# Kernel tuning notes

Hardware: AMD Instinct MI355X
Metric: run time of the kernel (lower is better)

Reference implementation:

```python
import jax, jax.numpy as jnp
import numpy as np

N, E, D, R = 8192, 131072, 128, 32
SIZES = (3, 5, 7)  # per-degree component counts (2l+1)
LN_EPS = 1e-5


def setup_inputs() -> dict:
    key = jax.random.key(0)
    ks = jax.random.split(key, 20)
    rn = lambda k, shape, s=1.0: jax.random.normal(k, shape, jnp.float32) * s
    inp = {
        'X0': rn(ks[0], (N, SIZES[0], D)),
        'X1': rn(ks[1], (N, SIZES[1], D)),
        'X2': rn(ks[2], (N, SIZES[2], D)),
        't_ij': rn(ks[3], (E, D)),
        'r0': rn(ks[4], (E, SIZES[0])),
        'r1': rn(ks[5], (E, SIZES[1])),
        'r2': rn(ks[6], (E, SIZES[2])),
        'edge_index': jax.random.randint(ks[7], (2, E), 0, N, dtype=jnp.int32),
        # params
        'W_vq': rn(ks[8], (D, R), D ** -0.5),
        'W_vk0': rn(ks[9], (D, R), D ** -0.5),
        'W_vk1': rn(ks[10], (D, R), D ** -0.5),
        'W_vk2': rn(ks[11], (D, R), D ** -0.5),
        'ln_g': jnp.ones((R,), jnp.float32),
        'ln_b': jnp.zeros((R,), jnp.float32),
        'W_w': rn(ks[12], (R, D), R ** -0.5),
        'b_w': jnp.zeros((D,), jnp.float32),
        'W_t1': rn(ks[13], (D, D), D ** -0.5),
        'b_t1': jnp.zeros((D,), jnp.float32),
        'W_t2': rn(ks[14], (D, D), D ** -0.5),
        'b_t2': jnp.zeros((D,), jnp.float32),
    }
    return inp


def _vec_rej(x, r):
    # x: [E, L, R], r: [E, L]; dot over component dim (L), keepdim, subtract projection
    r = r[..., None]
    dot = jnp.sum(x * r, axis=1, keepdims=True)  # [E, 1, R]
    return x - dot * r


def reference(X0, X1, X2, t_ij, r0, r1, r2, edge_index,
              W_vq, W_vk0, W_vk1, W_vk2, ln_g, ln_b, W_w, b_w,
              W_t1, b_t1, W_t2, b_t2):
    n_j, n_i = edge_index[0], edge_index[1]
    X_ls = jnp.concatenate([X0, X1, X2], axis=1)                 # [N, 15, D]
    eq_i = jnp.einsum('nld,dr->nlr', X_ls, W_vq)[n_i]            # [E, 15, R]
    ek = jnp.concatenate([
        jnp.einsum('nld,dr->nlr', X0, W_vk0),
        jnp.einsum('nld,dr->nlr', X1, W_vk1),
        jnp.einsum('nld,dr->nlr', X2, W_vk2)], axis=1)
    ek_j = ek[n_j]                                               # [E, 15, R]
    # per-degree vector rejection (vec_rej=True)
    qs, ksl, off = [], [], 0
    for r in (r0, r1, r2):
        s = r.shape[1]
        qs.append(_vec_rej(eq_i[:, off:off + s], r))
        ksl.append(_vec_rej(ek_j[:, off:off + s], -r))
        off += s
    eq_i = jnp.concatenate(qs, axis=1)
    ek_j = jnp.concatenate(ksl, axis=1)
    w_ij = jnp.sum(eq_i * ek_j, axis=1)                          # [E, R]
    # mlp_w = LayerNorm + Linear
    mu = jnp.mean(w_ij, axis=-1, keepdims=True)
    var = jnp.var(w_ij, axis=-1, keepdims=True)
    wn = (w_ij - mu) * jax.lax.rsqrt(var + LN_EPS) * ln_g + ln_b
    dw = wn @ W_w + b_w                                          # [E, D]
    # mlp_t = Linear -> silu -> Linear, then outer activation
    t = jax.nn.silu(t_ij @ W_t1 + b_t1) @ W_t2 + b_t2            # [E, D]
    return dw * jax.nn.silu(t)
```

## Files before the change

### kernel.cpp

```cpp
#include <hip/hip_runtime.h>
#include <hip/hip_bf16.h>

#define N_NODES 8192
#define N_EDGES 131072
#define LN_EPS  1e-5f

typedef __attribute__((ext_vector_type(8))) short bf16x8;
typedef __attribute__((ext_vector_type(4))) float f32x4;

__device__ __forceinline__ float silu_f(float x) {
    return x * __builtin_amdgcn_rcpf(1.0f + __expf(-x));
}

__device__ __forceinline__ unsigned short f2bf(float x) {
    union { float f; unsigned int u; } v; v.f = x;
    unsigned int r = v.u + 0x7FFFu + ((v.u >> 16) & 1u);
    return (unsigned short)(r >> 16);
}
__device__ __forceinline__ float bf2f(unsigned short u) {
    union { float f; unsigned int x; } v; v.x = ((unsigned int)u) << 16;
    return v.f;
}
__device__ __forceinline__ unsigned int pk2(float a, float b) {
    float2 t; t.x = a; t.y = b;
    union { __hip_bfloat162 h; unsigned int u; } v;
    v.h = __float22bfloat162_rn(t);
    return v.u;
}
__device__ __forceinline__ bf16x8 pack8(float4 u, float4 v) {
    union { bf16x8 b; unsigned int w[4]; } o;
    o.w[0] = pk2(u.x, u.y); o.w[1] = pk2(u.z, u.w);
    o.w[2] = pk2(v.x, v.y); o.w[3] = pk2(v.z, v.w);
    return o.b;
}
__device__ __forceinline__ f32x4 mfma16(bf16x8 a, bf16x8 b, f32x4 c) {
    return __builtin_amdgcn_mfma_f32_16x16x32_bf16(a, b, c, 0, 0, 0);
}

__global__ __launch_bounds__(256) void prep_kernel(
    const float* __restrict__ W_w, const float* __restrict__ W_t1,
    const float* __restrict__ W_t2, const float* __restrict__ Wvq,
    const float* __restrict__ Wvk0, const float* __restrict__ Wvk1,
    const float* __restrict__ Wvk2,
    unsigned short* __restrict__ Wtw, unsigned short* __restrict__ Wt1b,
    unsigned short* __restrict__ Wt2b, unsigned short* __restrict__ Wqt,
    unsigned short* __restrict__ Wk0t, unsigned short* __restrict__ Wk1t,
    unsigned short* __restrict__ Wk2t)
{
    int i = blockIdx.x * 256 + threadIdx.x;
    if (i < 16384) {
        int n = i >> 7, k = i & 127;
        Wt1b[i] = f2bf(W_t1[k * 128 + n]);
        Wt2b[i] = f2bf(W_t2[k * 128 + n]);
    }
    if (i < 4096) {
        { int n = i >> 5, k = i & 31; Wtw[i] = f2bf(W_w[k * 128 + n]); }
        int r = i >> 7, d = i & 127;
        Wqt[i]  = f2bf(Wvq [d * 32 + r]);
        Wk0t[i] = f2bf(Wvk0[d * 32 + r]);
        Wk1t[i] = f2bf(Wvk1[d * 32 + r]);
        Wk2t[i] = f2bf(Wvk2[d * 32 + r]);
    }
}

template<int S, int LOFF>
__device__ __forceinline__ void proj_body(
    const float* __restrict__ X, const unsigned short* __restrict__ Wqt,
    const unsigned short* __restrict__ Wkt,
    unsigned short* __restrict__ eq, unsigned short* __restrict__ ek,
    int row0)
{
    const int tid  = threadIdx.x;
    const int lane = tid & 63;
    const int wv   = tid >> 6;
    const int l15  = lane & 15;
    const int lk   = lane >> 4;
    const int xrow = row0 + wv * 16 + l15;

    bf16x8 xf[4];
    #pragma unroll
    for (int kt = 0; kt < 4; ++kt) {
        const float* p = X + (size_t)xrow * 128 + kt * 32 + lk * 8;
        xf[kt] = pack8(*(const float4*)p, *(const float4*)(p + 4));
    }

    f32x4 qa[2], ka[2];
    #pragma unroll
    for (int h = 0; h < 2; ++h) {
        qa[h] = (f32x4){0.f, 0.f, 0.f, 0.f};
        ka[h] = (f32x4){0.f, 0.f, 0.f, 0.f};
    }
    #pragma unroll
    for (int kt = 0; kt < 4; ++kt) {
        #pragma unroll
        for (int h = 0; h < 2; ++h) {
            bf16x8 wq = *(const bf16x8*)&Wqt[(h * 16 + l15) * 128 + kt * 32 + lk * 8];
            bf16x8 wk = *(const bf16x8*)&Wkt[(h * 16 + l15) * 128 + kt * 32 + lk * 8];
            qa[h] = mfma16(wq, xf[kt], qa[h]);
            ka[h] = mfma16(wk, xf[kt], ka[h]);
        }
    }

    const int n = xrow / S;
    const int l = xrow % S + LOFF;
    const size_t base = (size_t)n * 512 + l;
    #pragma unroll
    for (int h = 0; h < 2; ++h) {
        #pragma unroll
        for (int j = 0; j < 4; ++j) {
            const int r = h * 16 + lk * 4 + j;
            eq[base + r * 16] = f2bf(qa[h][j]);
            ek[base + r * 16] = f2bf(ka[h][j]);
        }
    }
}

__global__ __launch_bounds__(256) void proj_kernel(
    const float* __restrict__ X0, const float* __restrict__ X1,
    const float* __restrict__ X2,
    const unsigned short* __restrict__ Wqt,
    const unsigned short* __restrict__ Wk0t,
    const unsigned short* __restrict__ Wk1t,
    const unsigned short* __restrict__ Wk2t,
    unsigned short* __restrict__ eq, unsigned short* __restrict__ ek)
{
    const int b = blockIdx.x;
    if (b < 384)
        proj_body<3, 0>(X0, Wqt, Wk0t, eq, ek, b * 64);
    else if (b < 1024)
        proj_body<5, 3>(X1, Wqt, Wk1t, eq, ek, (b - 384) * 64);
    else
        proj_body<7, 8>(X2, Wqt, Wk2t, eq, ek, (b - 1024) * 64);
}

__global__ __launch_bounds__(256) void wn_kernel(
    const unsigned short* __restrict__ eq, const unsigned short* __restrict__ ek,
    const float* __restrict__ r0, const float* __restrict__ r1,
    const float* __restrict__ r2, const int* __restrict__ eidx,
    const float* __restrict__ ln_g, const float* __restrict__ ln_b,
    unsigned short* __restrict__ wn)
{
    const int tid = threadIdx.x;
    const int r   = tid & 31;
    const int e   = blockIdx.x * 8 + (tid >> 5);
    const float g  = ln_g[r];
    const float bb = ln_b[r];
    const int nj = eidx[e];
    const int ni = eidx[N_EDGES + e];

    const unsigned short* qp = eq + (size_t)ni * 512 + r * 16;
    const unsigned short* kp = ek + (size_t)nj * 512 + r * 16;
    bf16x8 q0 = *(const bf16x8*)qp;
    bf16x8 q1 = *(const bf16x8*)(qp + 8);
    bf16x8 k0 = *(const bf16x8*)kp;
    bf16x8 k1 = *(const bf16x8*)(kp + 8);

    float q[15], k[15], rv[15];
    #pragma unroll
    for (int l = 0; l < 8; ++l) {
        q[l] = bf2f((unsigned short)q0[l]);
        k[l] = bf2f((unsigned short)k0[l]);
    }
    #pragma unroll
    for (int l = 8; l < 15; ++l) {
        q[l] = bf2f((unsigned short)q1[l - 8]);
        k[l] = bf2f((unsigned short)k1[l - 8]);
    }
    #pragma unroll
    for (int c = 0; c < 3; ++c) rv[c]     = r0[e * 3 + c];
    #pragma unroll
    for (int c = 0; c < 5; ++c) rv[3 + c] = r1[e * 5 + c];
    #pragma unroll
    for (int c = 0; c < 7; ++c) rv[8 + c] = r2[e * 7 + c];

    float dq, dk;
    dq = q[0]*rv[0] + q[1]*rv[1] + q[2]*rv[2];
    dk = k[0]*rv[0] + k[1]*rv[1] + k[2]*rv[2];
    #pragma unroll
    for (int l = 0; l < 3; ++l) { q[l] -= dq * rv[l]; k[l] -= dk * rv[l]; }
    dq = 0.f; dk = 0.f;
    #pragma unroll
    for (int l = 3; l < 8; ++l) { dq += q[l]*rv[l]; dk += k[l]*rv[l]; }
    #pragma unroll
    for (int l = 3; l < 8; ++l) { q[l] -= dq * rv[l]; k[l] -= dk * rv[l]; }
    dq = 0.f; dk = 0.f;
    #pragma unroll
    for (int l = 8; l < 15; ++l) { dq += q[l]*rv[l]; dk += k[l]*rv[l]; }
    #pragma unroll
    for (int l = 8; l < 15; ++l) { q[l] -= dq * rv[l]; k[l] -= dk * rv[l]; }

    float w = 0.f;
    #pragma unroll
    for (int l = 0; l < 15; ++l) w = fmaf(q[l], k[l], w);

    float s = w, s2 = w * w;
    s += __shfl_xor(s, 1);  s2 += __shfl_xor(s2, 1);
    s += __shfl_xor(s, 2);  s2 += __shfl_xor(s2, 2);
    s += __shfl_xor(s, 4);  s2 += __shfl_xor(s2, 4);
    s += __shfl_xor(s, 8);  s2 += __shfl_xor(s2, 8);
    s += __shfl_xor(s, 16); s2 += __shfl_xor(s2, 16);
    const float mu  = s * (1.f / 32.f);
    const float var = s2 * (1.f / 32.f) - mu * mu;
    const float wnv = (w - mu) * rsqrtf(var + LN_EPS) * g + bb;
    wn[(size_t)e * 32 + r] = f2bf(wnv);
}

__global__ __launch_bounds__(256) void edge_kernel(
    const float* __restrict__ t_ij,
    const unsigned short* __restrict__ wn,
    const unsigned short* __restrict__ Wtw, const float* __restrict__ b_w,
    const unsigned short* __restrict__ Wt1, const float* __restrict__ b_t1,
    const unsigned short* __restrict__ Wt2, const float* __restrict__ b_t2,
    float* __restrict__ out)
{
    __shared__ __align__(16) unsigned short Hp[4][64 * 128];

    const int tid  = threadIdx.x;
    const int lane = tid & 63;
    const int wv   = tid >> 6;
    const int l15  = lane & 15;
    const int lk   = lane >> 4;
    const int tile = (blockIdx.x * 4 + wv) * 64;
    char* hp = (char*)&Hp[wv][0];
    const int swz = (l15 & 7) << 4;

    bf16x8 a1[4][4];
    #pragma unroll
    for (int kt = 0; kt < 4; ++kt)
        #pragma unroll
        for (int rt = 0; rt < 4; ++rt) {
            const float* p = t_ij + (size_t)(tile + rt * 16 + l15) * 128
                           + kt * 32 + lk * 8;
            a1[kt][rt] = pack8(*(const float4*)p, *(const float4*)(p + 4));
        }

    bf16x8 wnf[4];
    #pragma unroll
    for (int rt = 0; rt < 4; ++rt)
        wnf[rt] = *(const bf16x8*)&wn[(size_t)(tile + rt * 16 + l15) * 32 + lk * 8];

    #pragma unroll
    for (int ct = 0; ct < 8; ++ct) {
        bf16x8 w1f[4];
        #pragma unroll
        for (int kt = 0; kt < 4; ++kt)
            w1f[kt] = *(const bf16x8*)&Wt1[(size_t)(ct * 16 + l15) * 128
                                           + kt * 32 + lk * 8];
        f32x4 ac[4];
        #pragma unroll
        for (int rt = 0; rt < 4; ++rt) ac[rt] = (f32x4){0.f, 0.f, 0.f, 0.f};
        #pragma unroll
        for (int kt = 0; kt < 4; ++kt)
            #pragma unroll
            for (int rt = 0; rt < 4; ++rt)
                ac[rt] = mfma16(w1f[kt], a1[kt][rt], ac[rt]);

        const float4 bt1 = *(const float4*)&b_t1[ct * 16 + lk * 4];
        #pragma unroll
        for (int rt = 0; rt < 4; ++rt) {
            uint2 hh;
            hh.x = pk2(silu_f(ac[rt][0] + bt1.x), silu_f(ac[rt][1] + bt1.y));
            hh.y = pk2(silu_f(ac[rt][2] + bt1.z), silu_f(ac[rt][3] + bt1.w));
            *(uint2*)(hp + (((rt * 16 + l15) * 256 + ct * 32 + lk * 8) ^ swz)) = hh;
        }
    }

    bf16x8 a2[4][4];
    #pragma unroll
    for (int kt = 0; kt < 4; ++kt)
        #pragma unroll
        for (int rt = 0; rt < 4; ++rt)
            a2[kt][rt] = *(const bf16x8*)(hp +
                (((rt * 16 + l15) * 256 + kt * 64 + lk * 16) ^ swz));

    #pragma unroll
    for (int ct = 0; ct < 8; ++ct) {
        bf16x8 w2f[4];
        #pragma unroll
        for (int kt = 0; kt < 4; ++kt)
            w2f[kt] = *(const bf16x8*)&Wt2[(size_t)(ct * 16 + l15) * 128
                                           + kt * 32 + lk * 8];
        bf16x8 wwf = *(const bf16x8*)&Wtw[(ct * 16 + l15) * 32 + lk * 8];

        f32x4 o[4], d[4];
        #pragma unroll
        for (int rt = 0; rt < 4; ++rt) o[rt] = (f32x4){0.f, 0.f, 0.f, 0.f};
        #pragma unroll
        for (int kt = 0; kt < 4; ++kt)
            #pragma unroll
            for (int rt = 0; rt < 4; ++rt)
                o[rt] = mfma16(w2f[kt], a2[kt][rt], o[rt]);
        #pragma unroll
        for (int rt = 0; rt < 4; ++rt)
            d[rt] = mfma16(wwf, wnf[rt], (f32x4){0.f, 0.f, 0.f, 0.f});

        const float4 bwv = *(const float4*)&b_w[ct * 16 + lk * 4];
        const float4 b2v = *(const float4*)&b_t2[ct * 16 + lk * 4];
        #pragma unroll
        for (int rt = 0; rt < 4; ++rt) {
            float4 s;
            s.x = (d[rt][0] + bwv.x) * silu_f(o[rt][0] + b2v.x);
            s.y = (d[rt][1] + bwv.y) * silu_f(o[rt][1] + b2v.y);
            s.z = (d[rt][2] + bwv.z) * silu_f(o[rt][2] + b2v.z);
            s.w = (d[rt][3] + bwv.w) * silu_f(o[rt][3] + b2v.w);
            *(float4*)&out[(size_t)(tile + rt * 16 + l15) * 128 + ct * 16 + lk * 4] = s;
        }
    }
}

extern "C" void kernel_launch(void* const* d_in, const int* in_sizes, int n_in,
                              void* d_out, int out_size, void* d_ws, size_t ws_size,
                              hipStream_t stream) {
    (void)in_sizes; (void)n_in; (void)out_size; (void)ws_size;
    const float* X0   = (const float*)d_in[0];
    const float* X1   = (const float*)d_in[1];
    const float* X2   = (const float*)d_in[2];
    const float* t_ij = (const float*)d_in[3];
    const float* r0   = (const float*)d_in[4];
    const float* r1   = (const float*)d_in[5];
    const float* r2   = (const float*)d_in[6];
    const int*   eidx = (const int*)d_in[7];
    const float* Wvq  = (const float*)d_in[8];
    const float* Wvk0 = (const float*)d_in[9];
    const float* Wvk1 = (const float*)d_in[10];
    const float* Wvk2 = (const float*)d_in[11];
    const float* ln_g = (const float*)d_in[12];
    const float* ln_b = (const float*)d_in[13];
    const float* W_w  = (const float*)d_in[14];
    const float* b_w  = (const float*)d_in[15];
    const float* W_t1 = (const float*)d_in[16];
    const float* b_t1 = (const float*)d_in[17];
    const float* W_t2 = (const float*)d_in[18];
    const float* b_t2 = (const float*)d_in[19];
    float* out = (float*)d_out;

    unsigned short* eq   = (unsigned short*)d_ws;
    unsigned short* ek   = eq  + (size_t)N_NODES * 512;
    unsigned short* wn   = ek  + (size_t)N_NODES * 512;
    unsigned short* Wtw  = wn  + (size_t)N_EDGES * 32;
    unsigned short* Wt1b = Wtw  + 4096;
    unsigned short* Wt2b = Wt1b + 16384;
    unsigned short* Wqt  = Wt2b + 16384;
    unsigned short* Wk0t = Wqt  + 4096;
    unsigned short* Wk1t = Wk0t + 4096;
    unsigned short* Wk2t = Wk1t + 4096;

    prep_kernel<<<64, 256, 0, stream>>>(W_w, W_t1, W_t2, Wvq, Wvk0, Wvk1, Wvk2,
                                        Wtw, Wt1b, Wt2b, Wqt, Wk0t, Wk1t, Wk2t);
    proj_kernel<<<1920, 256, 0, stream>>>(X0, X1, X2, Wqt, Wk0t, Wk1t, Wk2t,
                                          eq, ek);
    wn_kernel<<<N_EDGES / 8, 256, 0, stream>>>(eq, ek, r0, r1, r2, eidx,
                                               ln_g, ln_b, wn);
    edge_kernel<<<N_EDGES / 256, 256, 0, stream>>>(t_ij, wn, Wtw, b_w,
                                                   Wt1b, b_t1, Wt2b, b_t2, out);
}
```

Measured before the change: 110.1 us.

## Fuse edge-weight LayerNorm into edge kernel with algebraic rejection and folded affine

Removes the separate wn kernel. Each lane of the edge kernel now gathers its own edge's full q and k rows and computes all 32 channel weights itself. The paired vector rejections are rewritten as qk - dq*dk*(2-|r|^2), so the rejected vectors are never formed. LayerNorm gain and bias are folded into the bf16 W_w matrix and a precomputed bias in the prep kernel. Normalized weights go through LDS into MFMA fragments, which removes the wn round-trip to global memory and one launch. The cost is higher register pressure (32 weights per lane), uncoalesced per-lane row gathers, and a serializing barrier before the t_ij loads.

```diff
diff --git a/kernel.cpp b/kernel.cpp
--- a/kernel.cpp
+++ b/kernel.cpp
@@ -41,11 +41,12 @@
     const float* __restrict__ W_w, const float* __restrict__ W_t1,
     const float* __restrict__ W_t2, const float* __restrict__ Wvq,
     const float* __restrict__ Wvk0, const float* __restrict__ Wvk1,
-    const float* __restrict__ Wvk2,
+    const float* __restrict__ Wvk2, const float* __restrict__ ln_g,
+    const float* __restrict__ ln_b, const float* __restrict__ b_w,
     unsigned short* __restrict__ Wtw, unsigned short* __restrict__ Wt1b,
     unsigned short* __restrict__ Wt2b, unsigned short* __restrict__ Wqt,
     unsigned short* __restrict__ Wk0t, unsigned short* __restrict__ Wk1t,
-    unsigned short* __restrict__ Wk2t)
+    unsigned short* __restrict__ Wk2t, float* __restrict__ bwf)
 {
     int i = blockIdx.x * 256 + threadIdx.x;
     if (i < 16384) {
@@ -54,12 +55,19 @@
         Wt2b[i] = f2bf(W_t2[k * 128 + n]);
     }
     if (i < 4096) {
-        { int n = i >> 5, k = i & 31; Wtw[i] = f2bf(W_w[k * 128 + n]); }
+        { int n = i >> 5, r = i & 31; Wtw[i] = f2bf(ln_g[r] * W_w[r * 128 + n]); }
         int r = i >> 7, d = i & 127;
         Wqt[i]  = f2bf(Wvq [d * 32 + r]);
         Wk0t[i] = f2bf(Wvk0[d * 32 + r]);
         Wk1t[i] = f2bf(Wvk1[d * 32 + r]);
         Wk2t[i] = f2bf(Wvk2[d * 32 + r]);
+    }
+    if (blockIdx.x == 0 && threadIdx.x < 128) {
+        const int n = threadIdx.x;
+        float acc = b_w[n];
+        #pragma unroll
+        for (int r = 0; r < 32; ++r) acc += ln_b[r] * W_w[r * 128 + n];
+        bwf[n] = acc;
     }
 }
 
@@ -133,82 +141,12 @@
         proj_body<7, 8>(X2, Wqt, Wk2t, eq, ek, (b - 1024) * 64);
 }
 
-__global__ __launch_bounds__(256) void wn_kernel(
+__global__ __launch_bounds__(256) void edge_kernel(
+    const float* __restrict__ t_ij,
     const unsigned short* __restrict__ eq, const unsigned short* __restrict__ ek,
     const float* __restrict__ r0, const float* __restrict__ r1,
     const float* __restrict__ r2, const int* __restrict__ eidx,
-    const float* __restrict__ ln_g, const float* __restrict__ ln_b,
-    unsigned short* __restrict__ wn)
-{
-    const int tid = threadIdx.x;
-    const int r   = tid & 31;
-    const int e   = blockIdx.x * 8 + (tid >> 5);
-    const float g  = ln_g[r];
-    const float bb = ln_b[r];
-    const int nj = eidx[e];
-    const int ni = eidx[N_EDGES + e];
-
-    const unsigned short* qp = eq + (size_t)ni * 512 + r * 16;
-    const unsigned short* kp = ek + (size_t)nj * 512 + r * 16;
-    bf16x8 q0 = *(const bf16x8*)qp;
-    bf16x8 q1 = *(const bf16x8*)(qp + 8);
-    bf16x8 k0 = *(const bf16x8*)kp;
-    bf16x8 k1 = *(const bf16x8*)(kp + 8);
-
-    float q[15], k[15], rv[15];
-    #pragma unroll
-    for (int l = 0; l < 8; ++l) {
-        q[l] = bf2f((unsigned short)q0[l]);
-        k[l] = bf2f((unsigned short)k0[l]);
-    }
-    #pragma unroll
-    for (int l = 8; l < 15; ++l) {
-        q[l] = bf2f((unsigned short)q1[l - 8]);
-        k[l] = bf2f((unsigned short)k1[l - 8]);
-    }
-    #pragma unroll
-    for (int c = 0; c < 3; ++c) rv[c]     = r0[e * 3 + c];
-    #pragma unroll
-    for (int c = 0; c < 5; ++c) rv[3 + c] = r1[e * 5 + c];
-    #pragma unroll
-    for (int c = 0; c < 7; ++c) rv[8 + c] = r2[e * 7 + c];
-
-    float dq, dk;
-    dq = q[0]*rv[0] + q[1]*rv[1] + q[2]*rv[2];
-    dk = k[0]*rv[0] + k[1]*rv[1] + k[2]*rv[2];
-    #pragma unroll
-    for (int l = 0; l < 3; ++l) { q[l] -= dq * rv[l]; k[l] -= dk * rv[l]; }
-    dq = 0.f; dk = 0.f;
-    #pragma unroll
-    for (int l = 3; l < 8; ++l) { dq += q[l]*rv[l]; dk += k[l]*rv[l]; }
-    #pragma unroll
-    for (int l = 3; l < 8; ++l) { q[l] -= dq * rv[l]; k[l] -= dk * rv[l]; }
-    dq = 0.f; dk = 0.f;
-    #pragma unroll
-    for (int l = 8; l < 15; ++l) { dq += q[l]*rv[l]; dk += k[l]*rv[l]; }
-    #pragma unroll
-    for (int l = 8; l < 15; ++l) { q[l] -= dq * rv[l]; k[l] -= dk * rv[l]; }
-
-    float w = 0.f;
-    #pragma unroll
-    for (int l = 0; l < 15; ++l) w = fmaf(q[l], k[l], w);
-
-    float s = w, s2 = w * w;
-    s += __shfl_xor(s, 1);  s2 += __shfl_xor(s2, 1);
-    s += __shfl_xor(s, 2);  s2 += __shfl_xor(s2, 2);
-    s += __shfl_xor(s, 4);  s2 += __shfl_xor(s2, 4);
-    s += __shfl_xor(s, 8);  s2 += __shfl_xor(s2, 8);
-    s += __shfl_xor(s, 16); s2 += __shfl_xor(s2, 16);
-    const float mu  = s * (1.f / 32.f);
-    const float var = s2 * (1.f / 32.f) - mu * mu;
-    const float wnv = (w - mu) * rsqrtf(var + LN_EPS) * g + bb;
-    wn[(size_t)e * 32 + r] = f2bf(wnv);
-}
-
-__global__ __launch_bounds__(256) void edge_kernel(
-    const float* __restrict__ t_ij,
-    const unsigned short* __restrict__ wn,
-    const unsigned short* __restrict__ Wtw, const float* __restrict__ b_w,
+    const unsigned short* __restrict__ Wtw, const float* __restrict__ bwf,
     const unsigned short* __restrict__ Wt1, const float* __restrict__ b_t1,
     const unsigned short* __restrict__ Wt2, const float* __restrict__ b_t2,
     float* __restrict__ out)
@@ -224,6 +162,80 @@
     char* hp = (char*)&Hp[wv][0];
     const int swz = (l15 & 7) << 4;
 
+    const int e  = tile + lane;
+    const int nj = eidx[e];
+    const int ni = eidx[N_EDGES + e];
+
+    float rv[15];
+    #pragma unroll
+    for (int c = 0; c < 3; ++c) rv[c]     = r0[e * 3 + c];
+    #pragma unroll
+    for (int c = 0; c < 5; ++c) rv[3 + c] = r1[e * 5 + c];
+    #pragma unroll
+    for (int c = 0; c < 7; ++c) rv[8 + c] = r2[e * 7 + c];
+    float c0 = 2.f, c1 = 2.f, c2 = 2.f;
+    #pragma unroll
+    for (int l = 0; l < 3; ++l)  c0 -= rv[l] * rv[l];
+    #pragma unroll
+    for (int l = 3; l < 8; ++l)  c1 -= rv[l] * rv[l];
+    #pragma unroll
+    for (int l = 8; l < 15; ++l) c2 -= rv[l] * rv[l];
+
+    const unsigned short* qbase = eq + (size_t)ni * 512;
+    const unsigned short* kbase = ek + (size_t)nj * 512;
+
+    float w[32];
+    #pragma unroll
+    for (int r = 0; r < 32; ++r) {
+        bf16x8 q0 = *(const bf16x8*)(qbase + r * 16);
+        bf16x8 q1 = *(const bf16x8*)(qbase + r * 16 + 8);
+        bf16x8 k0 = *(const bf16x8*)(kbase + r * 16);
+        bf16x8 k1 = *(const bf16x8*)(kbase + r * 16 + 8);
+        float qv[15], kv[15];
+        #pragma unroll
+        for (int l = 0; l < 8; ++l) {
+            qv[l] = bf2f((unsigned short)q0[l]);
+            kv[l] = bf2f((unsigned short)k0[l]);
+        }
+        #pragma unroll
+        for (int l = 8; l < 15; ++l) {
+            qv[l] = bf2f((unsigned short)q1[l - 8]);
+            kv[l] = bf2f((unsigned short)k1[l - 8]);
+        }
+        float qk = 0.f;
+        #pragma unroll
+        for (int l = 0; l < 15; ++l) qk = fmaf(qv[l], kv[l], qk);
+        float dq0 = 0.f, dk0 = 0.f, dq1 = 0.f, dk1 = 0.f, dq2 = 0.f, dk2 = 0.f;
+        #pragma unroll
+        for (int l = 0; l < 3; ++l)  { dq0 = fmaf(qv[l], rv[l], dq0); dk0 = fmaf(kv[l], rv[l], dk0); }
+        #pragma unroll
+        for (int l = 3; l < 8; ++l)  { dq1 = fmaf(qv[l], rv[l], dq1); dk1 = fmaf(kv[l], rv[l], dk1); }
+        #pragma unroll
+        for (int l = 8; l < 15; ++l) { dq2 = fmaf(qv[l], rv[l], dq2); dk2 = fmaf(kv[l], rv[l], dk2); }
+        w[r] = qk - dq0 * dk0 * c0 - dq1 * dk1 * c1 - dq2 * dk2 * c2;
+    }
+
+    float s = 0.f, s2 = 0.f;
+    #pragma unroll
+    for (int r = 0; r < 32; ++r) { s += w[r]; s2 += w[r] * w[r]; }
+    const float mu   = s * (1.f / 32.f);
+    const float var  = s2 * (1.f / 32.f) - mu * mu;
+    const float rstd = rsqrtf(var + LN_EPS);
+
+    #pragma unroll
+    for (int p = 0; p < 8; ++p) {
+        uint2 pp;
+        pp.x = pk2((w[4*p+0] - mu) * rstd, (w[4*p+1] - mu) * rstd);
+        pp.y = pk2((w[4*p+2] - mu) * rstd, (w[4*p+3] - mu) * rstd);
+        *(uint2*)(hp + lane * 80 + p * 8) = pp;
+    }
+    bf16x8 wnf[4];
+    #pragma unroll
+    for (int rt = 0; rt < 4; ++rt)
+        wnf[rt] = *(const bf16x8*)(hp + (rt * 16 + l15) * 80 + lk * 16);
+    asm volatile("s_waitcnt lgkmcnt(0)" ::: "memory");
+    __builtin_amdgcn_sched_barrier(0);
+
     bf16x8 a1[4][4];
     #pragma unroll
     for (int kt = 0; kt < 4; ++kt)
@@ -233,11 +245,6 @@
                            + kt * 32 + lk * 8;
             a1[kt][rt] = pack8(*(const float4*)p, *(const float4*)(p + 4));
         }
-
-    bf16x8 wnf[4];
-    #pragma unroll
-    for (int rt = 0; rt < 4; ++rt)
-        wnf[rt] = *(const bf16x8*)&wn[(size_t)(tile + rt * 16 + l15) * 32 + lk * 8];
 
     #pragma unroll
     for (int ct = 0; ct < 8; ++ct) {
@@ -294,16 +301,16 @@
         for (int rt = 0; rt < 4; ++rt)
             d[rt] = mfma16(wwf, wnf[rt], (f32x4){0.f, 0.f, 0.f, 0.f});
 
-        const float4 bwv = *(const float4*)&b_w[ct * 16 + lk * 4];
+        const float4 bwv = *(const float4*)&bwf[ct * 16 + lk * 4];
         const float4 b2v = *(const float4*)&b_t2[ct * 16 + lk * 4];
         #pragma unroll
         for (int rt = 0; rt < 4; ++rt) {
-            float4 s;
-            s.x = (d[rt][0] + bwv.x) * silu_f(o[rt][0] + b2v.x);
-            s.y = (d[rt][1] + bwv.y) * silu_f(o[rt][1] + b2v.y);
-            s.z = (d[rt][2] + bwv.z) * silu_f(o[rt][2] + b2v.z);
-            s.w = (d[rt][3] + bwv.w) * silu_f(o[rt][3] + b2v.w);
-            *(float4*)&out[(size_t)(tile + rt * 16 + l15) * 128 + ct * 16 + lk * 4] = s;
+            float4 so;
+            so.x = (d[rt][0] + bwv.x) * silu_f(o[rt][0] + b2v.x);
+            so.y = (d[rt][1] + bwv.y) * silu_f(o[rt][1] + b2v.y);
+            so.z = (d[rt][2] + bwv.z) * silu_f(o[rt][2] + b2v.z);
+            so.w = (d[rt][3] + bwv.w) * silu_f(o[rt][3] + b2v.w);
+            *(float4*)&out[(size_t)(tile + rt * 16 + l15) * 128 + ct * 16 + lk * 4] = so;
         }
     }
 }
@@ -336,21 +343,22 @@
 
     unsigned short* eq   = (unsigned short*)d_ws;
     unsigned short* ek   = eq  + (size_t)N_NODES * 512;
-    unsigned short* wn   = ek  + (size_t)N_NODES * 512;
-    unsigned short* Wtw  = wn  + (size_t)N_EDGES * 32;
+    unsigned short* Wtw  = ek  + (size_t)N_NODES * 512;
     unsigned short* Wt1b = Wtw  + 4096;
     unsigned short* Wt2b = Wt1b + 16384;
     unsigned short* Wqt  = Wt2b + 16384;
     unsigned short* Wk0t = Wqt  + 4096;
     unsigned short* Wk1t = Wk0t + 4096;
     unsigned short* Wk2t = Wk1t + 4096;
+    float*          bwf  = (float*)(Wk2t + 4096);
 
     prep_kernel<<<64, 256, 0, stream>>>(W_w, W_t1, W_t2, Wvq, Wvk0, Wvk1, Wvk2,
-                                        Wtw, Wt1b, Wt2b, Wqt, Wk0t, Wk1t, Wk2t);
+                                        ln_g, ln_b, b_w,
+                                        Wtw, Wt1b, Wt2b, Wqt, Wk0t, Wk1t, Wk2t,
+                                        bwf);
     proj_kernel<<<1920, 256, 0, stream>>>(X0, X1, X2, Wqt, Wk0t, Wk1t, Wk2t,
                                           eq, ek);
-    wn_kernel<<<N_EDGES / 8, 256, 0, stream>>>(eq, ek, r0, r1, r2, eidx,
-                                               ln_g, ln_b, wn);
-    edge_kernel<<<N_EDGES / 256, 256, 0, stream>>>(t_ij, wn, Wtw, b_w,
+    edge_kernel<<<N_EDGES / 256, 256, 0, stream>>>(t_ij, eq, ek, r0, r1, r2,
+                                                   eidx, Wtw, bwf,
                                                    Wt1b, b_t1, Wt2b, b_t2, out);
 }
```

Result: slower. 121.6 us (+10.5%).

## Use closed-form rejected dot product, two edges per thread, hoist MLP weights

Applied to the files above, without the earlier changes.

Replaces the per-degree vector rejection in wn_kernel with a closed-form expression, qk - (q·r)(k·r)(2-|r|^2), which avoids materialising rejected vectors. Each thread now handles two edges, to raise memory-level parallelism for the gathers, and the grid is halved to match. In edge_kernel, all W_t1 and W_t2 MFMA fragments are preloaded into registers before their loops, and launch bounds are set to two blocks per SM. This increases register pressure and may cause spills. The closed form also rounds slightly differently.

```diff
diff --git a/kernel.cpp b/kernel.cpp
--- a/kernel.cpp
+++ b/kernel.cpp
@@ -133,6 +133,40 @@
         proj_body<7, 8>(X2, Wqt, Wk2t, eq, ek, (b - 1024) * 64);
 }
 
+__device__ __forceinline__ float edge_w(
+    bf16x8 q0, bf16x8 q1, bf16x8 k0, bf16x8 k1, const float* rv)
+{
+    float qv[15], kv[15];
+    #pragma unroll
+    for (int l = 0; l < 8; ++l) {
+        qv[l] = bf2f((unsigned short)q0[l]);
+        kv[l] = bf2f((unsigned short)k0[l]);
+    }
+    #pragma unroll
+    for (int l = 8; l < 15; ++l) {
+        qv[l] = bf2f((unsigned short)q1[l - 8]);
+        kv[l] = bf2f((unsigned short)k1[l - 8]);
+    }
+    float qk = 0.f;
+    #pragma unroll
+    for (int l = 0; l < 15; ++l) qk = fmaf(qv[l], kv[l], qk);
+    float c0 = 2.f, c1 = 2.f, c2 = 2.f;
+    #pragma unroll
+    for (int l = 0; l < 3; ++l)  c0 -= rv[l] * rv[l];
+    #pragma unroll
+    for (int l = 3; l < 8; ++l)  c1 -= rv[l] * rv[l];
+    #pragma unroll
+    for (int l = 8; l < 15; ++l) c2 -= rv[l] * rv[l];
+    float dq0 = 0.f, dk0 = 0.f, dq1 = 0.f, dk1 = 0.f, dq2 = 0.f, dk2 = 0.f;
+    #pragma unroll
+    for (int l = 0; l < 3; ++l)  { dq0 = fmaf(qv[l], rv[l], dq0); dk0 = fmaf(kv[l], rv[l], dk0); }
+    #pragma unroll
+    for (int l = 3; l < 8; ++l)  { dq1 = fmaf(qv[l], rv[l], dq1); dk1 = fmaf(kv[l], rv[l], dk1); }
+    #pragma unroll
+    for (int l = 8; l < 15; ++l) { dq2 = fmaf(qv[l], rv[l], dq2); dk2 = fmaf(kv[l], rv[l], dk2); }
+    return qk - dq0 * dk0 * c0 - dq1 * dk1 * c1 - dq2 * dk2 * c2;
+}
+
 __global__ __launch_bounds__(256) void wn_kernel(
     const unsigned short* __restrict__ eq, const unsigned short* __restrict__ ek,
     const float* __restrict__ r0, const float* __restrict__ r1,
@@ -142,70 +176,50 @@
 {
     const int tid = threadIdx.x;
     const int r   = tid & 31;
-    const int e   = blockIdx.x * 8 + (tid >> 5);
+    const int hw  = tid >> 5;
+    const int e0  = blockIdx.x * 16 + hw * 2;
+    const int e1  = e0 + 1;
     const float g  = ln_g[r];
     const float bb = ln_b[r];
-    const int nj = eidx[e];
-    const int ni = eidx[N_EDGES + e];
-
-    const unsigned short* qp = eq + (size_t)ni * 512 + r * 16;
-    const unsigned short* kp = ek + (size_t)nj * 512 + r * 16;
-    bf16x8 q0 = *(const bf16x8*)qp;
-    bf16x8 q1 = *(const bf16x8*)(qp + 8);
-    bf16x8 k0 = *(const bf16x8*)kp;
-    bf16x8 k1 = *(const bf16x8*)(kp + 8);
-
-    float q[15], k[15], rv[15];
-    #pragma unroll
-    for (int l = 0; l < 8; ++l) {
-        q[l] = bf2f((unsigned short)q0[l]);
-        k[l] = bf2f((unsigned short)k0[l]);
-    }
-    #pragma unroll
-    for (int l = 8; l < 15; ++l) {
-        q[l] = bf2f((unsigned short)q1[l - 8]);
-        k[l] = bf2f((unsigned short)k1[l - 8]);
-    }
-    #pragma unroll
-    for (int c = 0; c < 3; ++c) rv[c]     = r0[e * 3 + c];
-    #pragma unroll
-    for (int c = 0; c < 5; ++c) rv[3 + c] = r1[e * 5 + c];
-    #pragma unroll
-    for (int c = 0; c < 7; ++c) rv[8 + c] = r2[e * 7 + c];
-
-    float dq, dk;
-    dq = q[0]*rv[0] + q[1]*rv[1] + q[2]*rv[2];
-    dk = k[0]*rv[0] + k[1]*rv[1] + k[2]*rv[2];
-    #pragma unroll
-    for (int l = 0; l < 3; ++l) { q[l] -= dq * rv[l]; k[l] -= dk * rv[l]; }
-    dq = 0.f; dk = 0.f;
-    #pragma unroll
-    for (int l = 3; l < 8; ++l) { dq += q[l]*rv[l]; dk += k[l]*rv[l]; }
-    #pragma unroll
-    for (int l = 3; l < 8; ++l) { q[l] -= dq * rv[l]; k[l] -= dk * rv[l]; }
-    dq = 0.f; dk = 0.f;
-    #pragma unroll
-    for (int l = 8; l < 15; ++l) { dq += q[l]*rv[l]; dk += k[l]*rv[l]; }
-    #pragma unroll
-    for (int l = 8; l < 15; ++l) { q[l] -= dq * rv[l]; k[l] -= dk * rv[l]; }
-
-    float w = 0.f;
-    #pragma unroll
-    for (int l = 0; l < 15; ++l) w = fmaf(q[l], k[l], w);
-
-    float s = w, s2 = w * w;
-    s += __shfl_xor(s, 1);  s2 += __shfl_xor(s2, 1);
-    s += __shfl_xor(s, 2);  s2 += __shfl_xor(s2, 2);
-    s += __shfl_xor(s, 4);  s2 += __shfl_xor(s2, 4);
-    s += __shfl_xor(s, 8);  s2 += __shfl_xor(s2, 8);
-    s += __shfl_xor(s, 16); s2 += __shfl_xor(s2, 16);
-    const float mu  = s * (1.f / 32.f);
-    const float var = s2 * (1.f / 32.f) - mu * mu;
-    const float wnv = (w - mu) * rsqrtf(var + LN_EPS) * g + bb;
-    wn[(size_t)e * 32 + r] = f2bf(wnv);
-}
-
-__global__ __launch_bounds__(256) void edge_kernel(
+
+    const int nj0 = eidx[e0], ni0 = eidx[N_EDGES + e0];
+    const int nj1 = eidx[e1], ni1 = eidx[N_EDGES + e1];
+
+    const unsigned short* qp0 = eq + (size_t)ni0 * 512 + r * 16;
+    const unsigned short* kp0 = ek + (size_t)nj0 * 512 + r * 16;
+    const unsigned short* qp1 = eq + (size_t)ni1 * 512 + r * 16;
+    const unsigned short* kp1 = ek + (size_t)nj1 * 512 + r * 16;
+    bf16x8 qa0 = *(const bf16x8*)qp0, qb0 = *(const bf16x8*)(qp0 + 8);
+    bf16x8 ka0 = *(const bf16x8*)kp0, kb0 = *(const bf16x8*)(kp0 + 8);
+    bf16x8 qa1 = *(const bf16x8*)qp1, qb1 = *(const bf16x8*)(qp1 + 8);
+    bf16x8 ka1 = *(const bf16x8*)kp1, kb1 = *(const bf16x8*)(kp1 + 8);
+
+    float rva[15], rvb[15];
+    #pragma unroll
+    for (int c = 0; c < 3; ++c) { rva[c]     = r0[e0 * 3 + c]; rvb[c]     = r0[e1 * 3 + c]; }
+    #pragma unroll
+    for (int c = 0; c < 5; ++c) { rva[3 + c] = r1[e0 * 5 + c]; rvb[3 + c] = r1[e1 * 5 + c]; }
+    #pragma unroll
+    for (int c = 0; c < 7; ++c) { rva[8 + c] = r2[e0 * 7 + c]; rvb[8 + c] = r2[e1 * 7 + c]; }
+
+    const float w0 = edge_w(qa0, qb0, ka0, kb0, rva);
+    const float w1 = edge_w(qa1, qb1, ka1, kb1, rvb);
+
+    float s0 = w0, s20 = w0 * w0, s1 = w1, s21 = w1 * w1;
+    #pragma unroll
+    for (int off = 1; off < 32; off <<= 1) {
+        s0  += __shfl_xor(s0,  off); s20 += __shfl_xor(s20, off);
+        s1  += __shfl_xor(s1,  off); s21 += __shfl_xor(s21, off);
+    }
+    const float mu0   = s0 * (1.f / 32.f);
+    const float var0  = s20 * (1.f / 32.f) - mu0 * mu0;
+    const float mu1   = s1 * (1.f / 32.f);
+    const float var1  = s21 * (1.f / 32.f) - mu1 * mu1;
+    wn[(size_t)e0 * 32 + r] = f2bf((w0 - mu0) * rsqrtf(var0 + LN_EPS) * g + bb);
+    wn[(size_t)e1 * 32 + r] = f2bf((w1 - mu1) * rsqrtf(var1 + LN_EPS) * g + bb);
+}
+
+__global__ __launch_bounds__(256, 2) void edge_kernel(
     const float* __restrict__ t_ij,
     const unsigned short* __restrict__ wn,
     const unsigned short* __restrict__ Wtw, const float* __restrict__ b_w,
@@ -239,13 +253,16 @@
     for (int rt = 0; rt < 4; ++rt)
         wnf[rt] = *(const bf16x8*)&wn[(size_t)(tile + rt * 16 + l15) * 32 + lk * 8];
 
+    bf16x8 w1f[8][4];
+    #pragma unroll
+    for (int ct = 0; ct < 8; ++ct)
+        #pragma unroll
+        for (int kt = 0; kt < 4; ++kt)
+            w1f[ct][kt] = *(const bf16x8*)&Wt1[(size_t)(ct * 16 + l15) * 128
+                                               + kt * 32 + lk * 8];
+
     #pragma unroll
     for (int ct = 0; ct < 8; ++ct) {
-        bf16x8 w1f[4];
-        #pragma unroll
-        for (int kt = 0; kt < 4; ++kt)
-            w1f[kt] = *(const bf16x8*)&Wt1[(size_t)(ct * 16 + l15) * 128
-                                           + kt * 32 + lk * 8];
         f32x4 ac[4];
         #pragma unroll
         for (int rt = 0; rt < 4; ++rt) ac[rt] = (f32x4){0.f, 0.f, 0.f, 0.f};
@@ -253,7 +270,7 @@
         for (int kt = 0; kt < 4; ++kt)
             #pragma unroll
             for (int rt = 0; rt < 4; ++rt)
-                ac[rt] = mfma16(w1f[kt], a1[kt][rt], ac[rt]);
+                ac[rt] = mfma16(w1f[ct][kt], a1[kt][rt], ac[rt]);
 
         const float4 bt1 = *(const float4*)&b_t1[ct * 16 + lk * 4];
         #pragma unroll
@@ -265,6 +282,14 @@
         }
     }
 
+    bf16x8 w2f[8][4];
+    #pragma unroll
+    for (int ct = 0; ct < 8; ++ct)
+        #pragma unroll
+        for (int kt = 0; kt < 4; ++kt)
+            w2f[ct][kt] = *(const bf16x8*)&Wt2[(size_t)(ct * 16 + l15) * 128
+                                               + kt * 32 + lk * 8];
+
     bf16x8 a2[4][4];
     #pragma unroll
     for (int kt = 0; kt < 4; ++kt)
@@ -275,11 +300,6 @@
 
     #pragma unroll
     for (int ct = 0; ct < 8; ++ct) {
-        bf16x8 w2f[4];
-        #pragma unroll
-        for (int kt = 0; kt < 4; ++kt)
-            w2f[kt] = *(const bf16x8*)&Wt2[(size_t)(ct * 16 + l15) * 128
-                                           + kt * 32 + lk * 8];
         bf16x8 wwf = *(const bf16x8*)&Wtw[(ct * 16 + l15) * 32 + lk * 8];
 
         f32x4 o[4], d[4];
@@ -289,7 +309,7 @@
         for (int kt = 0; kt < 4; ++kt)
             #pragma unroll
             for (int rt = 0; rt < 4; ++rt)
-                o[rt] = mfma16(w2f[kt], a2[kt][rt], o[rt]);
+                o[rt] = mfma16(w2f[ct][kt], a2[kt][rt], o[rt]);
         #pragma unroll
         for (int rt = 0; rt < 4; ++rt)
             d[rt] = mfma16(wwf, wnf[rt], (f32x4){0.f, 0.f, 0.f, 0.f});
@@ -349,8 +369,8 @@
                                         Wtw, Wt1b, Wt2b, Wqt, Wk0t, Wk1t, Wk2t);
     proj_kernel<<<1920, 256, 0, stream>>>(X0, X1, X2, Wqt, Wk0t, Wk1t, Wk2t,
                                           eq, ek);
-    wn_kernel<<<N_EDGES / 8, 256, 0, stream>>>(eq, ek, r0, r1, r2, eidx,
-                                               ln_g, ln_b, wn);
+    wn_kernel<<<N_EDGES / 16, 256, 0, stream>>>(eq, ek, r0, r1, r2, eidx,
+                                                ln_g, ln_b, wn);
     edge_kernel<<<N_EDGES / 256, 256, 0, stream>>>(t_ij, wn, Wtw, b_w,
                                                    Wt1b, b_t1, Wt2b, b_t2, out);
 }
```

New measurement: 111.4 us. No clear change (+1.2%).
